# Kernel tuning notes

Measured on AMD Instinct MI355X. Metric: run time of the kernel, lower is better.

The kernel has to match this reference:

```python
import jax, jax.numpy as jnp
import numpy as np

B, IN, N, E = 2048, 1024, 64, 128
NEG_SLOPE = 0.01  # torch LeakyReLU default

def setup_inputs() -> dict:
    key = jax.random.key(0)
    k = jax.random.split(key, 5)
    scale_in = 1.0 / np.sqrt(IN)
    scale_ctx = 1.0 / np.sqrt(2 * E)
    return {
        "x": jax.random.normal(k[0], (B, IN), dtype=jnp.float32),
        # stacked per-concept Linear(in_features, 2*emb_size)
        "W_ctx": jax.random.uniform(k[1], (N, IN, 2 * E), jnp.float32, -scale_in, scale_in),
        "b_ctx": jax.random.uniform(k[2], (N, 2 * E), jnp.float32, -scale_in, scale_in),
        # shared Linear(2*emb_size, 1)
        "w_prob": jax.random.uniform(k[3], (2 * E,), jnp.float32, -scale_ctx, scale_ctx),
        "b_prob": jax.random.uniform(k[4], (), jnp.float32, -scale_ctx, scale_ctx),
    }

def reference(x, W_ctx, b_ctx, w_prob, b_prob):
    # context: [B, N, 2E] = LeakyReLU(x @ W_i + b_i) for all concepts i at once
    ctx = jnp.einsum("bi,nio->bno", x, W_ctx) + b_ctx
    ctx = jnp.where(ctx >= 0, ctx, NEG_SLOPE * ctx)
    # shared gate: [B, N]
    c_pred = jax.nn.sigmoid(jnp.einsum("bno,o->bn", ctx, w_prob) + b_prob)
    # gated blend of positive/negative halves -> [B, N, E]
    p = c_pred[..., None]
    c_emb = ctx[..., :E] * p + ctx[..., E:] * (1.0 - p)
    return c_emb, c_pred
```

## Files before the change

### kernel.cpp

```cpp
#include <hip/hip_runtime.h>
#include <hip/hip_bf16.h>

typedef __attribute__((ext_vector_type(4))) short short4v;
typedef __attribute__((ext_vector_type(8))) short short8v;
typedef __attribute__((ext_vector_type(4))) float floatx4;

#define B_ROWS 2048
#define K_DIM  1024
#define N_CON  64
#define TWO_E  256
#define E_DIM  128
#define BM     64
#define BK     64
#define A_STRIDE 72
#define B_STRIDE 72
#define LDSA_BYTES (BM * A_STRIDE * 2)
#define LDSB_BYTES (TWO_E * B_STRIDE * 2)
#define SMEM_BYTES (LDSA_BYTES + LDSB_BYTES)
#define EMB_ELEMS 16777216ULL

static __device__ inline unsigned short bf16bits(float f) {
    __hip_bfloat16 h = __float2bfloat16(f);
    unsigned short u;
    __builtin_memcpy(&u, &h, 2);
    return u;
}

__global__ void __launch_bounds__(256) transpose_w(const float* __restrict__ W,
                                                   unsigned short* __restrict__ Wt) {
    __shared__ unsigned short t[64 * 68];
    const int tid = threadIdx.x;
    const int ot = blockIdx.x, ktile = blockIdx.y, n = blockIdx.z;
    const float* src = W + ((size_t)n * K_DIM + (size_t)ktile * 64) * TWO_E + ot * 64;
    unsigned short* dst = Wt + ((size_t)n * TWO_E + (size_t)ot * 64) * K_DIM + ktile * 64;

#pragma unroll
    for (int it = 0; it < 4; ++it) {
        int r = it * 16 + (tid >> 4);
        int c = (tid & 15) * 4;
        floatx4 v = *(const floatx4*)&src[(size_t)r * TWO_E + c];
        short4v b;
        b[0] = (short)bf16bits(v[0]);
        b[1] = (short)bf16bits(v[1]);
        b[2] = (short)bf16bits(v[2]);
        b[3] = (short)bf16bits(v[3]);
        *(short4v*)&t[r * 68 + c] = b;
    }
    __syncthreads();
#pragma unroll
    for (int it = 0; it < 4; ++it) {
        int o = it * 16 + (tid >> 4);
        int k = (tid & 15) * 4;
        short4v v;
#pragma unroll
        for (int j = 0; j < 4; ++j) v[j] = (short)t[(k + j) * 68 + o];
        *(short4v*)&dst[(size_t)o * K_DIM + k] = v;
    }
}

template <bool PRET>
__global__ void __launch_bounds__(256, 2)
concept_kernel(const float* __restrict__ x,
               const float* __restrict__ Wc,
               const unsigned short* __restrict__ Wt,
               const float* __restrict__ bc,
               const float* __restrict__ wp,
               const float* __restrict__ bp,
               float* __restrict__ out) {
    __shared__ __align__(16) char smem[SMEM_BYTES];
    unsigned short* ldsA = (unsigned short*)smem;
    unsigned short* ldsB = (unsigned short*)(smem + LDSA_BYTES);

    const int tid  = threadIdx.x;
    const int wave = tid >> 6;
    const int lane = tid & 63;
    const int lg   = lane >> 4;
    const int l15  = lane & 15;
    const int rb = blockIdx.x;
    const int n  = blockIdx.y;

    const float* xg = x + (size_t)rb * BM * K_DIM;

    floatx4 acc[4][4];
#pragma unroll
    for (int mi = 0; mi < 4; ++mi)
#pragma unroll
        for (int oi = 0; oi < 4; ++oi) acc[mi][oi] = (floatx4){0.f, 0.f, 0.f, 0.f};

    for (int kt = 0; kt < K_DIM; kt += BK) {
#pragma unroll
        for (int it = 0; it < 4; ++it) {
            int q = it * 256 + tid;
            int r = q >> 4, c = (q & 15) * 4;
            floatx4 v = *(const floatx4*)&xg[(size_t)r * K_DIM + kt + c];
            short4v b;
            b[0] = (short)bf16bits(v[0]);
            b[1] = (short)bf16bits(v[1]);
            b[2] = (short)bf16bits(v[2]);
            b[3] = (short)bf16bits(v[3]);
            *(short4v*)&ldsA[r * A_STRIDE + c] = b;
        }
        if (PRET) {
            const unsigned short* wtg = Wt + (size_t)n * TWO_E * K_DIM;
#pragma unroll
            for (int it = 0; it < 8; ++it) {
                int q = it * 256 + tid;
                int o = q >> 3, ck = q & 7;
                short8v v = *(const short8v*)&wtg[(size_t)o * K_DIM + kt + ck * 8];
                *(short8v*)&ldsB[o * B_STRIDE + ck * 8] = v;
            }
        } else {
            const float* wg = Wc + (size_t)n * K_DIM * TWO_E;
#pragma unroll
            for (int it = 0; it < 8; ++it) {
                short8v v;
#pragma unroll
                for (int j = 0; j < 8; ++j)
                    v[j] = (short)bf16bits(wg[(size_t)(kt + it * 8 + j) * TWO_E + tid]);
                *(short8v*)&ldsB[tid * B_STRIDE + it * 8] = v;
            }
        }
        __syncthreads();

#pragma unroll
        for (int ks = 0; ks < 2; ++ks) {
            const int kof = ks * 32 + lg * 8;
            short8v af[4], bfr[4];
#pragma unroll
            for (int mi = 0; mi < 4; ++mi)
                af[mi] = *(short8v*)&ldsA[(mi * 16 + l15) * A_STRIDE + kof];
#pragma unroll
            for (int oi = 0; oi < 4; ++oi)
                bfr[oi] = *(short8v*)&ldsB[(wave * 64 + oi * 16 + l15) * B_STRIDE + kof];
#pragma unroll
            for (int mi = 0; mi < 4; ++mi)
#pragma unroll
                for (int oi = 0; oi < 4; ++oi)
                    acc[mi][oi] = __builtin_amdgcn_mfma_f32_16x16x32_bf16(
                        af[mi], bfr[oi], acc[mi][oi], 0, 0, 0);
        }
        __syncthreads();
    }

    float biasf[4], wpf[4];
#pragma unroll
    for (int oi = 0; oi < 4; ++oi) {
        int o = wave * 64 + oi * 16 + l15;
        biasf[oi] = bc[n * TWO_E + o];
        wpf[oi]  = wp[o];
    }
#pragma unroll
    for (int mi = 0; mi < 4; ++mi)
#pragma unroll
        for (int oi = 0; oi < 4; ++oi)
#pragma unroll
            for (int j = 0; j < 4; ++j) {
                float v = acc[mi][oi][j] + biasf[oi];
                acc[mi][oi][j] = v >= 0.f ? v : 0.01f * v;
            }

    float* eneg    = (float*)smem;
    float* partial = (float*)(smem + 33792);
    float* pv      = (float*)(smem + 34816);

    if (wave >= 2) {
#pragma unroll
        for (int mi = 0; mi < 4; ++mi)
#pragma unroll
            for (int oi = 0; oi < 4; ++oi)
#pragma unroll
                for (int j = 0; j < 4; ++j) {
                    int row = mi * 16 + lg * 4 + j;
                    int e = (wave - 2) * 64 + oi * 16 + l15;
                    eneg[row * 132 + e] = acc[mi][oi][j];
                }
    }
#pragma unroll
    for (int mi = 0; mi < 4; ++mi)
#pragma unroll
        for (int j = 0; j < 4; ++j) {
            float ps = 0.f;
#pragma unroll
            for (int oi = 0; oi < 4; ++oi) ps += acc[mi][oi][j] * wpf[oi];
            ps += __shfl_xor(ps, 1);
            ps += __shfl_xor(ps, 2);
            ps += __shfl_xor(ps, 4);
            ps += __shfl_xor(ps, 8);
            if (l15 == 0) partial[(mi * 16 + lg * 4 + j) * 4 + wave] = ps;
        }
    __syncthreads();

    if (tid < 64) {
        float s = partial[tid * 4] + partial[tid * 4 + 1] + partial[tid * 4 + 2] +
                  partial[tid * 4 + 3] + bp[0];
        float p = 1.f / (1.f + __expf(-s));
        pv[tid] = p;
        size_t bi = (size_t)rb * BM + tid;
        out[EMB_ELEMS + bi * N_CON + n] = p;
    }
    __syncthreads();

    if (wave < 2) {
#pragma unroll
        for (int mi = 0; mi < 4; ++mi)
#pragma unroll
            for (int oi = 0; oi < 4; ++oi)
#pragma unroll
                for (int j = 0; j < 4; ++j) {
                    int row = mi * 16 + lg * 4 + j;
                    int e = wave * 64 + oi * 16 + l15;
                    float p = pv[row];
                    float v = acc[mi][oi][j] * p + eneg[row * 132 + e] * (1.f - p);
                    size_t bi = (size_t)rb * BM + row;
                    out[(bi * N_CON + n) * E_DIM + e] = v;
                }
    }
}

extern "C" void kernel_launch(void* const* d_in, const int* in_sizes, int n_in,
                              void* d_out, int out_size, void* d_ws, size_t ws_size,
                              hipStream_t stream) {
    const float* x  = (const float*)d_in[0];
    const float* Wc = (const float*)d_in[1];
    const float* bc = (const float*)d_in[2];
    const float* wp = (const float*)d_in[3];
    const float* bp = (const float*)d_in[4];
    float* out = (float*)d_out;

    const size_t wt_bytes = (size_t)N_CON * K_DIM * TWO_E * 2;
    if (ws_size >= wt_bytes) {
        unsigned short* Wt = (unsigned short*)d_ws;
        transpose_w<<<dim3(4, 16, 64), 256, 0, stream>>>(Wc, Wt);
        concept_kernel<true><<<dim3(32, 64), 256, 0, stream>>>(x, Wc, Wt, bc, wp, bp, out);
    } else {
        concept_kernel<false><<<dim3(32, 64), 256, 0, stream>>>(x, Wc, nullptr, bc, wp, bp, out);
    }
}
```

Before: 217.4 us.

## Double row tile to 128 with 8 waves and pair pos/neg columns per wave

The GEMM block now covers 128 batch rows with 512 threads, so each staged weight tile is reused across twice as many rows and fewer blocks reload the same weights. Output columns are assigned so that each wave holds both the positive and the negative half for the same embedding columns, which lets the gated blend happen in registers and removes the LDS round trip for the negative half. The weight transpose kernel is also rewritten to pack bf16 pairs into 32-bit LDS words and write 16-byte stores. In exchange there are half as many blocks, which lowers parallelism across the GPU, and the launch bound asks for four 512-thread blocks per CU, which may add register pressure.

Result: faster. 205.3 us (-5.6%).

```diff
diff --git a/kernel.cpp b/kernel.cpp
--- a/kernel.cpp
+++ b/kernel.cpp
@@ -10,7 +10,7 @@
 #define N_CON  64
 #define TWO_E  256
 #define E_DIM  128
-#define BM     64
+#define BM     128
 #define BK     64
 #define A_STRIDE 72
 #define B_STRIDE 72
@@ -28,38 +28,38 @@
 
 __global__ void __launch_bounds__(256) transpose_w(const float* __restrict__ W,
                                                    unsigned short* __restrict__ Wt) {
-    __shared__ unsigned short t[64 * 68];
+    __shared__ unsigned int lds2[64 * 36];
     const int tid = threadIdx.x;
     const int ot = blockIdx.x, ktile = blockIdx.y, n = blockIdx.z;
     const float* src = W + ((size_t)n * K_DIM + (size_t)ktile * 64) * TWO_E + ot * 64;
     unsigned short* dst = Wt + ((size_t)n * TWO_E + (size_t)ot * 64) * K_DIM + ktile * 64;
 
-#pragma unroll
-    for (int it = 0; it < 4; ++it) {
-        int r = it * 16 + (tid >> 4);
-        int c = (tid & 15) * 4;
-        floatx4 v = *(const floatx4*)&src[(size_t)r * TWO_E + c];
-        short4v b;
-        b[0] = (short)bf16bits(v[0]);
-        b[1] = (short)bf16bits(v[1]);
-        b[2] = (short)bf16bits(v[2]);
-        b[3] = (short)bf16bits(v[3]);
-        *(short4v*)&t[r * 68 + c] = b;
+    const int kp = tid >> 4;
+    const int c  = (tid & 15) * 4;
+#pragma unroll
+    for (int it = 0; it < 2; ++it) {
+        const int k0 = it * 32 + kp * 2;
+        floatx4 r0 = *(const floatx4*)&src[(size_t)k0 * TWO_E + c];
+        floatx4 r1 = *(const floatx4*)&src[(size_t)(k0 + 1) * TWO_E + c];
+#pragma unroll
+        for (int j = 0; j < 4; ++j) {
+            unsigned int d = (unsigned int)bf16bits(r0[j]) |
+                             ((unsigned int)bf16bits(r1[j]) << 16);
+            lds2[(c + j) * 36 + it * 16 + kp] = d;
+        }
     }
     __syncthreads();
 #pragma unroll
-    for (int it = 0; it < 4; ++it) {
-        int o = it * 16 + (tid >> 4);
-        int k = (tid & 15) * 4;
-        short4v v;
-#pragma unroll
-        for (int j = 0; j < 4; ++j) v[j] = (short)t[(k + j) * 68 + o];
-        *(short4v*)&dst[(size_t)o * K_DIM + k] = v;
+    for (int it = 0; it < 2; ++it) {
+        int q = it * 256 + tid;
+        int o = q >> 3, kc = q & 7;
+        short8v v = *(short8v*)&lds2[o * 36 + kc * 4];
+        *(short8v*)&dst[(size_t)o * K_DIM + kc * 8] = v;
     }
 }
 
 template <bool PRET>
-__global__ void __launch_bounds__(256, 2)
+__global__ void __launch_bounds__(512, 4)
 concept_kernel(const float* __restrict__ x,
                const float* __restrict__ Wc,
                const unsigned short* __restrict__ Wt,
@@ -76,9 +76,15 @@
     const int lane = tid & 63;
     const int lg   = lane >> 4;
     const int l15  = lane & 15;
+    const int h    = wave >> 2;
+    const int og   = wave & 3;
     const int rb = blockIdx.x;
     const int n  = blockIdx.y;
 
+    int otile[4];
+#pragma unroll
+    for (int oi = 0; oi < 4; ++oi) otile[oi] = og * 32 + (oi & 1) * 16 + (oi & 2) * 64;
+
     const float* xg = x + (size_t)rb * BM * K_DIM;
 
     floatx4 acc[4][4];
@@ -90,7 +96,7 @@
     for (int kt = 0; kt < K_DIM; kt += BK) {
 #pragma unroll
         for (int it = 0; it < 4; ++it) {
-            int q = it * 256 + tid;
+            int q = it * 512 + tid;
             int r = q >> 4, c = (q & 15) * 4;
             floatx4 v = *(const floatx4*)&xg[(size_t)r * K_DIM + kt + c];
             short4v b;
@@ -103,21 +109,23 @@
         if (PRET) {
             const unsigned short* wtg = Wt + (size_t)n * TWO_E * K_DIM;
 #pragma unroll
-            for (int it = 0; it < 8; ++it) {
-                int q = it * 256 + tid;
+            for (int it = 0; it < 4; ++it) {
+                int q = it * 512 + tid;
                 int o = q >> 3, ck = q & 7;
                 short8v v = *(const short8v*)&wtg[(size_t)o * K_DIM + kt + ck * 8];
                 *(short8v*)&ldsB[o * B_STRIDE + ck * 8] = v;
             }
         } else {
-            const float* wg = Wc + (size_t)n * K_DIM * TWO_E;
-#pragma unroll
-            for (int it = 0; it < 8; ++it) {
-                short8v v;
-#pragma unroll
-                for (int j = 0; j < 8; ++j)
-                    v[j] = (short)bf16bits(wg[(size_t)(kt + it * 8 + j) * TWO_E + tid]);
-                *(short8v*)&ldsB[tid * B_STRIDE + it * 8] = v;
+            if (tid < 256) {
+                const float* wg = Wc + (size_t)n * K_DIM * TWO_E;
+#pragma unroll
+                for (int it = 0; it < 8; ++it) {
+                    short8v v;
+#pragma unroll
+                    for (int j = 0; j < 8; ++j)
+                        v[j] = (short)bf16bits(wg[(size_t)(kt + it * 8 + j) * TWO_E + tid]);
+                    *(short8v*)&ldsB[tid * B_STRIDE + it * 8] = v;
+                }
             }
         }
         __syncthreads();
@@ -128,10 +136,10 @@
             short8v af[4], bfr[4];
 #pragma unroll
             for (int mi = 0; mi < 4; ++mi)
-                af[mi] = *(short8v*)&ldsA[(mi * 16 + l15) * A_STRIDE + kof];
+                af[mi] = *(short8v*)&ldsA[(h * 64 + mi * 16 + l15) * A_STRIDE + kof];
 #pragma unroll
             for (int oi = 0; oi < 4; ++oi)
-                bfr[oi] = *(short8v*)&ldsB[(wave * 64 + oi * 16 + l15) * B_STRIDE + kof];
+                bfr[oi] = *(short8v*)&ldsB[(otile[oi] + l15) * B_STRIDE + kof];
 #pragma unroll
             for (int mi = 0; mi < 4; ++mi)
 #pragma unroll
@@ -145,7 +153,7 @@
     float biasf[4], wpf[4];
 #pragma unroll
     for (int oi = 0; oi < 4; ++oi) {
-        int o = wave * 64 + oi * 16 + l15;
+        int o = otile[oi] + l15;
         biasf[oi] = bc[n * TWO_E + o];
         wpf[oi]  = wp[o];
     }
@@ -159,22 +167,9 @@
                 acc[mi][oi][j] = v >= 0.f ? v : 0.01f * v;
             }
 
-    float* eneg    = (float*)smem;
-    float* partial = (float*)(smem + 33792);
-    float* pv      = (float*)(smem + 34816);
-
-    if (wave >= 2) {
-#pragma unroll
-        for (int mi = 0; mi < 4; ++mi)
-#pragma unroll
-            for (int oi = 0; oi < 4; ++oi)
-#pragma unroll
-                for (int j = 0; j < 4; ++j) {
-                    int row = mi * 16 + lg * 4 + j;
-                    int e = (wave - 2) * 64 + oi * 16 + l15;
-                    eneg[row * 132 + e] = acc[mi][oi][j];
-                }
-    }
+    float* partial = (float*)smem;
+    float* pv      = (float*)(smem + 2048);
+
 #pragma unroll
     for (int mi = 0; mi < 4; ++mi)
 #pragma unroll
@@ -186,11 +181,11 @@
             ps += __shfl_xor(ps, 2);
             ps += __shfl_xor(ps, 4);
             ps += __shfl_xor(ps, 8);
-            if (l15 == 0) partial[(mi * 16 + lg * 4 + j) * 4 + wave] = ps;
+            if (l15 == 0) partial[(h * 64 + mi * 16 + lg * 4 + j) * 4 + og] = ps;
         }
     __syncthreads();
 
-    if (tid < 64) {
+    if (tid < 128) {
         float s = partial[tid * 4] + partial[tid * 4 + 1] + partial[tid * 4 + 2] +
                   partial[tid * 4 + 3] + bp[0];
         float p = 1.f / (1.f + __expf(-s));
@@ -200,21 +195,19 @@
     }
     __syncthreads();
 
-    if (wave < 2) {
-#pragma unroll
-        for (int mi = 0; mi < 4; ++mi)
-#pragma unroll
-            for (int oi = 0; oi < 4; ++oi)
-#pragma unroll
-                for (int j = 0; j < 4; ++j) {
-                    int row = mi * 16 + lg * 4 + j;
-                    int e = wave * 64 + oi * 16 + l15;
-                    float p = pv[row];
-                    float v = acc[mi][oi][j] * p + eneg[row * 132 + e] * (1.f - p);
-                    size_t bi = (size_t)rb * BM + row;
-                    out[(bi * N_CON + n) * E_DIM + e] = v;
-                }
-    }
+#pragma unroll
+    for (int mi = 0; mi < 4; ++mi)
+#pragma unroll
+        for (int oi = 0; oi < 2; ++oi)
+#pragma unroll
+            for (int j = 0; j < 4; ++j) {
+                int row = h * 64 + mi * 16 + lg * 4 + j;
+                int e = og * 32 + oi * 16 + l15;
+                float p = pv[row];
+                float v = acc[mi][oi][j] * p + acc[mi][oi + 2][j] * (1.f - p);
+                size_t bi = (size_t)rb * BM + row;
+                out[(bi * N_CON + n) * E_DIM + e] = v;
+            }
 }
 
 extern "C" void kernel_launch(void* const* d_in, const int* in_sizes, int n_in,
@@ -231,8 +224,8 @@
     if (ws_size >= wt_bytes) {
         unsigned short* Wt = (unsigned short*)d_ws;
         transpose_w<<<dim3(4, 16, 64), 256, 0, stream>>>(Wc, Wt);
-        concept_kernel<true><<<dim3(32, 64), 256, 0, stream>>>(x, Wc, Wt, bc, wp, bp, out);
+        concept_kernel<true><<<dim3(16, 64), 512, 0, stream>>>(x, Wc, Wt, bc, wp, bp, out);
     } else {
-        concept_kernel<false><<<dim3(32, 64), 256, 0, stream>>>(x, Wc, nullptr, bc, wp, bp, out);
-    }
-}
+        concept_kernel<false><<<dim3(16, 64), 512, 0, stream>>>(x, Wc, nullptr, bc, wp, bp, out);
+    }
+}
```
